# Performance work log

Measured on AMD Instinct MI355X. Metric: run time of the kernel, lower is better.

Reference implementation:

```python
import jax, jax.numpy as jnp
import numpy as np

B, S, E, H = 2, 2048, 1024, 16
DH = E // H
SCALE = DH ** -0.5

def setup_inputs() -> dict:
    key = jax.random.key(0)
    ks = jax.random.split(key, 5)
    w_std = (2.0 / (E + E)) ** 0.5  # xavier-ish scale
    return {
        'x': jax.random.normal(ks[0], (B, S, E), jnp.float32),
        'Wq': jax.random.normal(ks[1], (E, E), jnp.float32) * w_std,
        'bq': jnp.zeros((E,), jnp.float32),
        'Wk': jax.random.normal(ks[2], (E, E), jnp.float32) * w_std,
        'bk': jnp.zeros((E,), jnp.float32),
        'Wv': jax.random.normal(ks[3], (E, E), jnp.float32) * w_std,
        'bv': jnp.zeros((E,), jnp.float32),
        'Wo': jax.random.normal(ks[4], (E, E), jnp.float32) * w_std,
        'bo': jnp.zeros((E,), jnp.float32),
    }

def reference(x, Wq, bq, Wk, bk, Wv, bv, Wo, bo):
    # self-attention: query = key = value = x; torch Linear: y = x @ W.T + b
    q = (x @ Wq.T + bq) * SCALE            # [B,S,E]
    k = x @ Wk.T + bk
    v = x @ Wv.T + bv
    # split heads -> [B,S,H,DH]
    q = q.reshape(B, S, H, DH)
    k = k.reshape(B, S, H, DH)
    v = v.reshape(B, S, H, DH)
    # explicit attention matrix [B,H,S,S] (faithful to unfused bmm path)
    scores = jnp.einsum('bqhd,bkhd->bhqk', q, k)
    probs = jax.nn.softmax(scores, axis=-1)
    attn = jnp.einsum('bhqk,bkhd->bqhd', probs, v).reshape(B, S, E)
    return attn @ Wo.T + bo                # [B,S,E]
```

## Files before the change

kernel.cpp:

```cpp
#include <hip/hip_runtime.h>
#include <stdint.h>

#define BB 2
#define SS 2048
#define EE 1024
#define HH 16
#define DHD 64
#define MM (BB*SS)
#define QSCALE (0.125f * 1.4426950408889634f)

typedef __bf16 bf16;
typedef __bf16 bf16x8 __attribute__((ext_vector_type(8)));
typedef __bf16 bf16x4 __attribute__((ext_vector_type(4)));
typedef float  f32x4  __attribute__((ext_vector_type(4)));
typedef unsigned short ushort8 __attribute__((ext_vector_type(8)));

#define MFMA16(a,b,c) __builtin_amdgcn_mfma_f32_16x16x32_bf16(a,b,c,0,0,0)

__device__ __forceinline__ void gload_lds16(const void* g, void* l) {
  __builtin_amdgcn_global_load_lds(
      (const __attribute__((address_space(1))) unsigned int*)g,
      (__attribute__((address_space(3))) unsigned int*)l, 16, 0, 0);
}

__device__ __forceinline__ unsigned short f2bf(float f) {
  union { float f; unsigned u; } v; v.f = f;
  return (unsigned short)((v.u + 0x7FFFu + ((v.u >> 16) & 1u)) >> 16);
}

__global__ void convert_kernel(const float* __restrict__ x,
                               const float* __restrict__ wq, const float* __restrict__ wk,
                               const float* __restrict__ wv, const float* __restrict__ wo,
                               unsigned short* __restrict__ xbf,
                               unsigned short* __restrict__ wqb, unsigned short* __restrict__ wkb,
                               unsigned short* __restrict__ wvb, unsigned short* __restrict__ wob) {
  long t = (long)blockIdx.x * blockDim.x + threadIdx.x;
  long base = t * 8;
  const float* src; unsigned short* dst; long off;
  if (base < 4194304L) { src = x; dst = xbf; off = base; }
  else {
    long r = base - 4194304L; int j = (int)(r >> 20); off = r & 1048575L;
    src = (j==0)?wq:(j==1)?wk:(j==2)?wv:wo;
    dst = (j==0)?wqb:(j==1)?wkb:(j==2)?wvb:wob;
  }
  const float4* s4 = (const float4*)(src + off);
  float4 a = s4[0], b = s4[1];
  ushort8 o;
  o[0]=f2bf(a.x); o[1]=f2bf(a.y); o[2]=f2bf(a.z); o[3]=f2bf(a.w);
  o[4]=f2bf(b.x); o[5]=f2bf(b.y); o[6]=f2bf(b.z); o[7]=f2bf(b.w);
  *(ushort8*)(dst + off) = o;
}

#define G_STAGE(kbuf, kt) { \
    const size_t kb_ = (size_t)(kt) * 64; \
    char* d_ = lds + (kbuf) * 16384 + tid * 16; \
    gload_lds16(a0 + kb_, d_); \
    gload_lds16(a1 + kb_, d_ + 4096); \
    gload_lds16(b0 + kb_, d_ + 8192); \
    gload_lds16(b1 + kb_, d_ + 12288); \
  }

__global__ __launch_bounds__(256) void qkv_gemm(
    const bf16* __restrict__ xbf,
    const bf16* __restrict__ wqb, const bf16* __restrict__ wkb, const bf16* __restrict__ wvb,
    const float* __restrict__ bq, const float* __restrict__ bk, const float* __restrict__ bv,
    bf16* __restrict__ Q, bf16* __restrict__ K, bf16* __restrict__ VT) {
  __shared__ char lds[32768] __attribute__((aligned(16)));
  const int tid = threadIdx.x;
  const int bm = blockIdx.y * 128;
  const int bnG = blockIdx.x * 128;
  const int proj = bnG >> 10;
  const int bn = bnG & 1023;
  const bf16* wsel = (proj==0)?wqb:(proj==1)?wkb:wvb;
  const float* bias = (proj==0)?bq:(proj==1)?bk:bv;

  const int lane = tid & 63, w = tid >> 6;
  const int wm = (w>>1)*64, wn = (w&1)*64;
  const int c = lane & 15, g = lane >> 4;

  const int sr = tid >> 2;
  const int scb = ((tid & 3) * 16) ^ ((sr & 3) << 4);
  const char* a0 = (const char*)xbf  + ((size_t)(bm + sr     ) * 1024) * 2 + scb;
  const char* a1 = (const char*)xbf  + ((size_t)(bm + 64 + sr) * 1024) * 2 + scb;
  const char* b0 = (const char*)wsel + ((size_t)(bn + sr     ) * 1024) * 2 + scb;
  const char* b1 = (const char*)wsel + ((size_t)(bn + 64 + sr) * 1024) * 2 + scb;

  int aoff[4], boff[4];
#pragma unroll
  for (int mt=0; mt<4; ++mt) { int rr = wm + mt*16 + c; aoff[mt] = rr*64 + ((g*16) ^ ((rr&3)<<4)); }
#pragma unroll
  for (int nt=0; nt<4; ++nt) { int rr = wn + nt*16 + c; boff[nt] = 8192 + rr*64 + ((g*16) ^ ((rr&3)<<4)); }

  f32x4 acc[4][4];
#pragma unroll
  for (int mt=0; mt<4; ++mt)
#pragma unroll
    for (int nt=0; nt<4; ++nt) acc[mt][nt] = (f32x4){0.f,0.f,0.f,0.f};

  G_STAGE(0, 0);
  for (int kt = 0; kt < 32; ++kt) {
    const int cur = kt & 1;
    if (kt < 31) {
      G_STAGE(cur ^ 1, kt + 1);
      asm volatile("s_waitcnt vmcnt(4)" ::: "memory");
    } else {
      asm volatile("s_waitcnt vmcnt(0)" ::: "memory");
    }
    __builtin_amdgcn_s_barrier();
    const char* Ts = lds + cur * 16384;
    bf16x8 af[4], bfv[4];
#pragma unroll
    for (int mt=0; mt<4; ++mt) af[mt] = *(const bf16x8*)(Ts + aoff[mt]);
#pragma unroll
    for (int nt=0; nt<4; ++nt) bfv[nt] = *(const bf16x8*)(Ts + boff[nt]);
#pragma unroll
    for (int mt=0; mt<4; ++mt)
#pragma unroll
      for (int nt=0; nt<4; ++nt)
        acc[mt][nt] = MFMA16(af[mt], bfv[nt], acc[mt][nt]);
    asm volatile("s_waitcnt lgkmcnt(0)" ::: "memory");
    __builtin_amdgcn_s_barrier();
  }

  const int bidx = bm >> 11;
  const int srow = bm & 2047;
#pragma unroll
  for (int nt=0; nt<4; ++nt) {
    const int n = bn + wn + nt*16 + c;
    const float bv_ = bias[n];
    const int h = n >> 6, d = n & 63;
#pragma unroll
    for (int mt=0; mt<4; ++mt) {
      f32x4 a = acc[mt][nt];
      const int m0 = wm + mt*16 + g*4;
      if (proj == 0) {
#pragma unroll
        for (int r=0;r<4;++r) {
          int s = srow + m0 + r;
          Q[(((size_t)(bidx*16 + h))*2048 + s)*64 + d] = (bf16)((a[r] + bv_) * QSCALE);
        }
      } else if (proj == 1) {
#pragma unroll
        for (int r=0;r<4;++r) {
          int s = srow + m0 + r;
          K[(((size_t)(bidx*16 + h))*2048 + s)*64 + d] = (bf16)(a[r] + bv_);
        }
      } else {
        bf16x4 pk;
#pragma unroll
        for (int r=0;r<4;++r) pk[r] = (bf16)(a[r] + bv_);
        *(bf16x4*)(VT + (((size_t)(bidx*16 + h))*64 + d)*2048 + (srow + m0)) = pk;
      }
    }
  }
}

__global__ __launch_bounds__(256) void attn_kernel(
    const bf16* __restrict__ Q, const bf16* __restrict__ K,
    const bf16* __restrict__ VT, bf16* __restrict__ attn_out) {
  __shared__ char alds[32768] __attribute__((aligned(16)));
  const int tid = threadIdx.x;
  const int lane = tid & 63, w = tid >> 6;
  const int c = lane & 15, g = lane >> 4;
  const int x7 = c & 7;
  const int bh = blockIdx.y;
  const int qb = blockIdx.x * 64 + w * 16;
  const bf16* Qh = Q + (size_t)bh * 2048 * 64;
  const char* Khb = (const char*)(K  + (size_t)bh * 2048 * 64);
  const char* Vhb = (const char*)(VT + (size_t)bh * 64 * 2048);

  const int srow = tid >> 3, schunk = tid & 7;
  const int ssw = ((schunk ^ (srow & 7)) << 4);
  const char* srcK = Khb + (size_t)srow * 128  + ssw;
  const char* srcV = Vhb + (size_t)srow * 4096 + ssw;

#define ATT_STAGE(buf, kv) { \
    const char* sk_ = srcK + (size_t)(kv) * 128; \
    const char* sv_ = srcV + (size_t)(kv) * 2; \
    char* d_ = alds + (buf) * 16384 + tid * 16; \
    gload_lds16(sk_,            d_); \
    gload_lds16(sk_ + 32*128,   d_ + 4096); \
    gload_lds16(sv_,            d_ + 8192); \
    gload_lds16(sv_ + 32*4096,  d_ + 12288); \
  }

  bf16x8 qf0 = *(const bf16x8*)(Qh + (size_t)(qb + c)*64 + g*8);
  bf16x8 qf1 = *(const bf16x8*)(Qh + (size_t)(qb + c)*64 + 32 + g*8);

  f32x4 o[4];
#pragma unroll
  for (int dt=0; dt<4; ++dt) o[dt] = (f32x4){0.f,0.f,0.f,0.f};
  float m = -1e30f, l = 0.f;

  ATT_STAGE(0, 0);
  for (int t = 0; t < 32; ++t) {
    const int cur = t & 1;
    if (t < 31) {
      ATT_STAGE(cur ^ 1, (t + 1) * 64);
      asm volatile("s_waitcnt vmcnt(4)" ::: "memory");
    } else {
      asm volatile("s_waitcnt vmcnt(0)" ::: "memory");
    }
    __builtin_amdgcn_s_barrier();

    const char* Kl = alds + cur * 16384;
    const char* Vl = Kl + 8192;

    f32x4 st[4];
    __builtin_amdgcn_s_setprio(1);
#pragma unroll
    for (int ks = 0; ks < 4; ++ks) {
      const char* kr = Kl + (ks*16 + c) * 128;
      bf16x8 k0 = *(const bf16x8*)(kr + (((g    ) ^ x7) << 4));
      bf16x8 k1 = *(const bf16x8*)(kr + (((g + 4) ^ x7) << 4));
      f32x4 z = (f32x4){0.f,0.f,0.f,0.f};
      z = MFMA16(k0, qf0, z);
      z = MFMA16(k1, qf1, z);
      st[ks] = z;
    }
    __builtin_amdgcn_s_setprio(0);

    float m0_ = fmaxf(fmaxf(st[0][0], st[0][1]), st[0][2]);
    float m1_ = fmaxf(fmaxf(st[0][3], st[1][0]), st[1][1]);
    float m2_ = fmaxf(fmaxf(st[1][2], st[1][3]), st[2][0]);
    float m3_ = fmaxf(fmaxf(st[2][1], st[2][2]), st[2][3]);
    float m4_ = fmaxf(fmaxf(st[3][0], st[3][1]), st[3][2]);
    float tmax = fmaxf(fmaxf(fmaxf(m0_, m1_), m2_), fmaxf(fmaxf(m3_, m4_), st[3][3]));
    tmax = fmaxf(tmax, __shfl_xor(tmax, 16, 64));
    tmax = fmaxf(tmax, __shfl_xor(tmax, 32, 64));

    float p[4][4]; float ps = 0.f;
    if (__all(tmax <= m + 8.f)) {
#pragma unroll
      for (int ks = 0; ks < 4; ++ks)
#pragma unroll
        for (int r = 0; r < 4; ++r) { p[ks][r] = __builtin_exp2f(st[ks][r] - m); ps += p[ks][r]; }
      ps += __shfl_xor(ps, 16, 64);
      ps += __shfl_xor(ps, 32, 64);
      l += ps;
    } else {
      const float mnew = fmaxf(m, tmax);
      const float corr = __builtin_exp2f(m - mnew);
#pragma unroll
      for (int ks = 0; ks < 4; ++ks)
#pragma unroll
        for (int r = 0; r < 4; ++r) { p[ks][r] = __builtin_exp2f(st[ks][r] - mnew); ps += p[ks][r]; }
      ps += __shfl_xor(ps, 16, 64);
      ps += __shfl_xor(ps, 32, 64);
      l = l * corr + ps;
      m = mnew;
#pragma unroll
      for (int dt=0; dt<4; ++dt) o[dt] *= corr;
    }

    bf16x8 pfA, pfB;
#pragma unroll
    for (int r = 0; r < 4; ++r) {
      pfA[r] = (bf16)p[0][r]; pfA[4+r] = (bf16)p[1][r];
      pfB[r] = (bf16)p[2][r]; pfB[4+r] = (bf16)p[3][r];
    }

    const int i8 = (g & 1) * 8, gh = g >> 1;
    __builtin_amdgcn_s_setprio(1);
#pragma unroll
    for (int dt = 0; dt < 4; ++dt) {
      const char* vr = Vl + (dt*16 + c) * 128;
      bf16x4 va0 = *(const bf16x4*)(vr + (((gh    ) ^ x7) << 4) + i8);
      bf16x4 va1 = *(const bf16x4*)(vr + (((gh + 2) ^ x7) << 4) + i8);
      bf16x4 vb0 = *(const bf16x4*)(vr + (((gh + 4) ^ x7) << 4) + i8);
      bf16x4 vb1 = *(const bf16x4*)(vr + (((gh + 6) ^ x7) << 4) + i8);
      bf16x8 vfA = __builtin_shufflevector(va0, va1, 0,1,2,3,4,5,6,7);
      bf16x8 vfB = __builtin_shufflevector(vb0, vb1, 0,1,2,3,4,5,6,7);
      o[dt] = MFMA16(vfA, pfA, o[dt]);
      o[dt] = MFMA16(vfB, pfB, o[dt]);
    }
    __builtin_amdgcn_s_setprio(0);

    asm volatile("s_waitcnt lgkmcnt(0)" ::: "memory");
    __builtin_amdgcn_s_barrier();
  }
#undef ATT_STAGE

  const float inv = 1.0f / l;
  const int srow_q = qb + c;
  const int b = bh >> 4, h = bh & 15;
  bf16* outrow = attn_out + ((size_t)(b*2048 + srow_q))*1024 + h*64;
#pragma unroll
  for (int dt=0; dt<4; ++dt) {
    bf16x4 ov;
#pragma unroll
    for (int r=0;r<4;++r) ov[r] = (bf16)(o[dt][r] * inv);
    *(bf16x4*)(outrow + dt*16 + g*4) = ov;
  }
}

__global__ __launch_bounds__(256) void out_gemm(
    const bf16* __restrict__ A, const bf16* __restrict__ W,
    const float* __restrict__ bias, float* __restrict__ out) {
  __shared__ char lds[32768] __attribute__((aligned(16)));
  const int tid = threadIdx.x;
  const int bm = blockIdx.y * 128, bn = blockIdx.x * 128;
  const int lane = tid & 63, w = tid >> 6;
  const int wm = (w>>1)*64, wn = (w&1)*64;
  const int c = lane & 15, g = lane >> 4;

  const int sr = tid >> 2;
  const int scb = ((tid & 3) * 16) ^ ((sr & 3) << 4);
  const char* a0 = (const char*)A + ((size_t)(bm + sr     ) * 1024) * 2 + scb;
  const char* a1 = (const char*)A + ((size_t)(bm + 64 + sr) * 1024) * 2 + scb;
  const char* b0 = (const char*)W + ((size_t)(bn + sr     ) * 1024) * 2 + scb;
  const char* b1 = (const char*)W + ((size_t)(bn + 64 + sr) * 1024) * 2 + scb;

  int aoff[4], boff[4];
#pragma unroll
  for (int mt=0; mt<4; ++mt) { int rr = wm + mt*16 + c; aoff[mt] = rr*64 + ((g*16) ^ ((rr&3)<<4)); }
#pragma unroll
  for (int nt=0; nt<4; ++nt) { int rr = wn + nt*16 + c; boff[nt] = 8192 + rr*64 + ((g*16) ^ ((rr&3)<<4)); }

  f32x4 acc[4][4];
#pragma unroll
  for (int mt=0; mt<4; ++mt)
#pragma unroll
    for (int nt=0; nt<4; ++nt) acc[mt][nt] = (f32x4){0.f,0.f,0.f,0.f};

  G_STAGE(0, 0);
  for (int kt = 0; kt < 32; ++kt) {
    const int cur = kt & 1;
    if (kt < 31) {
      G_STAGE(cur ^ 1, kt + 1);
      asm volatile("s_waitcnt vmcnt(4)" ::: "memory");
    } else {
      asm volatile("s_waitcnt vmcnt(0)" ::: "memory");
    }
    __builtin_amdgcn_s_barrier();
    const char* Ts = lds + cur * 16384;
    bf16x8 af[4], bfv[4];
#pragma unroll
    for (int mt=0; mt<4; ++mt) af[mt] = *(const bf16x8*)(Ts + aoff[mt]);
#pragma unroll
    for (int nt=0; nt<4; ++nt) bfv[nt] = *(const bf16x8*)(Ts + boff[nt]);
#pragma unroll
    for (int mt=0; mt<4; ++mt)
#pragma unroll
      for (int nt=0; nt<4; ++nt)
        acc[mt][nt] = MFMA16(af[mt], bfv[nt], acc[mt][nt]);
    asm volatile("s_waitcnt lgkmcnt(0)" ::: "memory");
    __builtin_amdgcn_s_barrier();
  }

#pragma unroll
  for (int nt=0; nt<4; ++nt) {
    const int n = bn + wn + nt*16 + c;
    const float bv_ = bias[n];
#pragma unroll
    for (int mt=0; mt<4; ++mt) {
      const int m0 = bm + wm + mt*16 + g*4;
#pragma unroll
      for (int r=0;r<4;++r) out[(size_t)(m0 + r)*1024 + n] = acc[mt][nt][r] + bv_;
    }
  }
}

extern "C" void kernel_launch(void* const* d_in, const int* in_sizes, int n_in,
                              void* d_out, int out_size, void* d_ws, size_t ws_size,
                              hipStream_t stream) {
  const float* x  = (const float*)d_in[0];
  const float* Wq = (const float*)d_in[1];
  const float* bq = (const float*)d_in[2];
  const float* Wk = (const float*)d_in[3];
  const float* bk = (const float*)d_in[4];
  const float* Wv = (const float*)d_in[5];
  const float* bv = (const float*)d_in[6];
  const float* Wo = (const float*)d_in[7];
  const float* bo = (const float*)d_in[8];

  char* ws = (char*)d_ws;
  const size_t MiB = 1u << 20;
  unsigned short* xbf = (unsigned short*)(ws);
  unsigned short* wqb = (unsigned short*)(ws +  8*MiB);
  unsigned short* wkb = (unsigned short*)(ws + 10*MiB);
  unsigned short* wvb = (unsigned short*)(ws + 12*MiB);
  unsigned short* wob = (unsigned short*)(ws + 14*MiB);
  bf16* Qb    = (bf16*)(ws + 16*MiB);
  bf16* Kb    = (bf16*)(ws + 24*MiB);
  bf16* VTb   = (bf16*)(ws + 32*MiB);
  bf16* attnb = (bf16*)(ws + 40*MiB);

  convert_kernel<<<4096, 256, 0, stream>>>(x, Wq, Wk, Wv, Wo, xbf, wqb, wkb, wvb, wob);
  qkv_gemm<<<dim3(24, 32), 256, 0, stream>>>(
      (const bf16*)xbf, (const bf16*)wqb, (const bf16*)wkb, (const bf16*)wvb,
      bq, bk, bv, Qb, Kb, VTb);
  attn_kernel<<<dim3(32, 32), 256, 0, stream>>>(Qb, Kb, VTb, attnb);
  out_gemm<<<dim3(8, 32), 256, 0, stream>>>(attnb, (const bf16*)wob, bo, (float*)d_out);
}
```

Measured before the change: 239.5 us.

## Swap MFMA operands for vectorized Q/K/out stores; simplify online softmax

Swapping the A/B operands of the MFMA in the Q/K projection and output GEMMs transposes the accumulator layout, so each lane holds four consecutive columns. That allows packed bf16x4 stores for Q/K and float4 stores for the output, with float4 bias loads, instead of scattered scalar stores. The attention kernel drops the lazy-rescale branch and always rescales, and removes the s_setprio hints. The K-loop is factored into a shared template. The unconditional rescale adds multiply work per tile, and removing setprio may change how waves interleave.

```diff
diff --git a/kernel.cpp b/kernel.cpp
--- a/kernel.cpp
+++ b/kernel.cpp
@@ -51,7 +51,7 @@
   *(ushort8*)(dst + off) = o;
 }
 
-#define G_STAGE(kbuf, kt) { \
+#define GS_STAGE(kbuf, kt) { \
     const size_t kb_ = (size_t)(kt) * 64; \
     char* d_ = lds + (kbuf) * 16384 + tid * 16; \
     gload_lds16(a0 + kb_, d_); \
@@ -59,6 +59,38 @@
     gload_lds16(b0 + kb_, d_ + 8192); \
     gload_lds16(b1 + kb_, d_ + 12288); \
   }
+
+template<bool SWAP>
+__device__ __forceinline__ void gemm_kloop(
+    const char* a0, const char* a1, const char* b0, const char* b1,
+    char* lds, const int tid, const int (&aoff)[4], const int (&boff)[4],
+    f32x4 (&acc)[4][4]) {
+  GS_STAGE(0, 0);
+  for (int kt = 0; kt < 32; ++kt) {
+    const int cur = kt & 1;
+    if (kt < 31) {
+      GS_STAGE(cur ^ 1, kt + 1);
+      asm volatile("s_waitcnt vmcnt(4)" ::: "memory");
+    } else {
+      asm volatile("s_waitcnt vmcnt(0)" ::: "memory");
+    }
+    __builtin_amdgcn_s_barrier();
+    const char* Ts = lds + cur * 16384;
+    bf16x8 af[4], bfv[4];
+#pragma unroll
+    for (int mt=0; mt<4; ++mt) af[mt] = *(const bf16x8*)(Ts + aoff[mt]);
+#pragma unroll
+    for (int nt=0; nt<4; ++nt) bfv[nt] = *(const bf16x8*)(Ts + boff[nt]);
+#pragma unroll
+    for (int mt=0; mt<4; ++mt)
+#pragma unroll
+      for (int nt=0; nt<4; ++nt)
+        acc[mt][nt] = SWAP ? MFMA16(bfv[nt], af[mt], acc[mt][nt])
+                           : MFMA16(af[mt], bfv[nt], acc[mt][nt]);
+    asm volatile("s_waitcnt lgkmcnt(0)" ::: "memory");
+    __builtin_amdgcn_s_barrier();
+  }
+}
 
 __global__ __launch_bounds__(256) void qkv_gemm(
     const bf16* __restrict__ xbf,
@@ -97,58 +129,42 @@
 #pragma unroll
     for (int nt=0; nt<4; ++nt) acc[mt][nt] = (f32x4){0.f,0.f,0.f,0.f};
 
-  G_STAGE(0, 0);
-  for (int kt = 0; kt < 32; ++kt) {
-    const int cur = kt & 1;
-    if (kt < 31) {
-      G_STAGE(cur ^ 1, kt + 1);
-      asm volatile("s_waitcnt vmcnt(4)" ::: "memory");
-    } else {
-      asm volatile("s_waitcnt vmcnt(0)" ::: "memory");
-    }
-    __builtin_amdgcn_s_barrier();
-    const char* Ts = lds + cur * 16384;
-    bf16x8 af[4], bfv[4];
-#pragma unroll
-    for (int mt=0; mt<4; ++mt) af[mt] = *(const bf16x8*)(Ts + aoff[mt]);
-#pragma unroll
-    for (int nt=0; nt<4; ++nt) bfv[nt] = *(const bf16x8*)(Ts + boff[nt]);
-#pragma unroll
-    for (int mt=0; mt<4; ++mt)
-#pragma unroll
-      for (int nt=0; nt<4; ++nt)
-        acc[mt][nt] = MFMA16(af[mt], bfv[nt], acc[mt][nt]);
-    asm volatile("s_waitcnt lgkmcnt(0)" ::: "memory");
-    __builtin_amdgcn_s_barrier();
-  }
-
   const int bidx = bm >> 11;
   const int srow = bm & 2047;
-#pragma unroll
-  for (int nt=0; nt<4; ++nt) {
-    const int n = bn + wn + nt*16 + c;
-    const float bv_ = bias[n];
-    const int h = n >> 6, d = n & 63;
-#pragma unroll
-    for (int mt=0; mt<4; ++mt) {
-      f32x4 a = acc[mt][nt];
-      const int m0 = wm + mt*16 + g*4;
-      if (proj == 0) {
-#pragma unroll
-        for (int r=0;r<4;++r) {
-          int s = srow + m0 + r;
-          Q[(((size_t)(bidx*16 + h))*2048 + s)*64 + d] = (bf16)((a[r] + bv_) * QSCALE);
-        }
-      } else if (proj == 1) {
-#pragma unroll
-        for (int r=0;r<4;++r) {
-          int s = srow + m0 + r;
-          K[(((size_t)(bidx*16 + h))*2048 + s)*64 + d] = (bf16)(a[r] + bv_);
-        }
-      } else {
+
+  if (proj != 2) {
+    gemm_kloop<true>(a0, a1, b0, b1, lds, tid, aoff, boff, acc);
+    bf16* dst = (proj == 0) ? Q : K;
+    const float qs = (proj == 0) ? QSCALE : 1.0f;
+#pragma unroll
+    for (int nt=0; nt<4; ++nt) {
+      const int n0 = bn + wn + nt*16 + g*4;
+      const float4 b4 = *(const float4*)(bias + n0);
+      const int h = n0 >> 6, d0 = n0 & 63;
+#pragma unroll
+      for (int mt=0; mt<4; ++mt) {
+        const int s = srow + wm + mt*16 + c;
         bf16x4 pk;
-#pragma unroll
-        for (int r=0;r<4;++r) pk[r] = (bf16)(a[r] + bv_);
+        pk[0] = (bf16)((acc[mt][nt][0] + b4.x) * qs);
+        pk[1] = (bf16)((acc[mt][nt][1] + b4.y) * qs);
+        pk[2] = (bf16)((acc[mt][nt][2] + b4.z) * qs);
+        pk[3] = (bf16)((acc[mt][nt][3] + b4.w) * qs);
+        *(bf16x4*)(dst + (((size_t)(bidx*16 + h))*2048 + s)*64 + d0) = pk;
+      }
+    }
+  } else {
+    gemm_kloop<false>(a0, a1, b0, b1, lds, tid, aoff, boff, acc);
+#pragma unroll
+    for (int nt=0; nt<4; ++nt) {
+      const int n = bn + wn + nt*16 + c;
+      const float bv_ = bias[n];
+      const int h = n >> 6, d = n & 63;
+#pragma unroll
+      for (int mt=0; mt<4; ++mt) {
+        const int m0 = wm + mt*16 + g*4;
+        bf16x4 pk;
+#pragma unroll
+        for (int r=0;r<4;++r) pk[r] = (bf16)(acc[mt][nt][r] + bv_);
         *(bf16x4*)(VT + (((size_t)(bidx*16 + h))*64 + d)*2048 + (srow + m0)) = pk;
       }
     }
@@ -207,7 +223,6 @@
     const char* Vl = Kl + 8192;
 
     f32x4 st[4];
-    __builtin_amdgcn_s_setprio(1);
 #pragma unroll
     for (int ks = 0; ks < 4; ++ks) {
       const char* kr = Kl + (ks*16 + c) * 128;
@@ -218,40 +233,26 @@
       z = MFMA16(k1, qf1, z);
       st[ks] = z;
     }
-    __builtin_amdgcn_s_setprio(0);
-
-    float m0_ = fmaxf(fmaxf(st[0][0], st[0][1]), st[0][2]);
-    float m1_ = fmaxf(fmaxf(st[0][3], st[1][0]), st[1][1]);
-    float m2_ = fmaxf(fmaxf(st[1][2], st[1][3]), st[2][0]);
-    float m3_ = fmaxf(fmaxf(st[2][1], st[2][2]), st[2][3]);
-    float m4_ = fmaxf(fmaxf(st[3][0], st[3][1]), st[3][2]);
-    float tmax = fmaxf(fmaxf(fmaxf(m0_, m1_), m2_), fmaxf(fmaxf(m3_, m4_), st[3][3]));
+
+    float tmax = -1e30f;
+#pragma unroll
+    for (int ks = 0; ks < 4; ++ks)
+      tmax = fmaxf(tmax, fmaxf(fmaxf(st[ks][0], st[ks][1]), fmaxf(st[ks][2], st[ks][3])));
     tmax = fmaxf(tmax, __shfl_xor(tmax, 16, 64));
     tmax = fmaxf(tmax, __shfl_xor(tmax, 32, 64));
-
+    const float mnew = fmaxf(m, tmax);
+    const float corr = __builtin_exp2f(m - mnew);
     float p[4][4]; float ps = 0.f;
-    if (__all(tmax <= m + 8.f)) {
-#pragma unroll
-      for (int ks = 0; ks < 4; ++ks)
-#pragma unroll
-        for (int r = 0; r < 4; ++r) { p[ks][r] = __builtin_exp2f(st[ks][r] - m); ps += p[ks][r]; }
-      ps += __shfl_xor(ps, 16, 64);
-      ps += __shfl_xor(ps, 32, 64);
-      l += ps;
-    } else {
-      const float mnew = fmaxf(m, tmax);
-      const float corr = __builtin_exp2f(m - mnew);
-#pragma unroll
-      for (int ks = 0; ks < 4; ++ks)
-#pragma unroll
-        for (int r = 0; r < 4; ++r) { p[ks][r] = __builtin_exp2f(st[ks][r] - mnew); ps += p[ks][r]; }
-      ps += __shfl_xor(ps, 16, 64);
-      ps += __shfl_xor(ps, 32, 64);
-      l = l * corr + ps;
-      m = mnew;
-#pragma unroll
-      for (int dt=0; dt<4; ++dt) o[dt] *= corr;
-    }
+#pragma unroll
+    for (int ks = 0; ks < 4; ++ks)
+#pragma unroll
+      for (int r = 0; r < 4; ++r) { p[ks][r] = __builtin_exp2f(st[ks][r] - mnew); ps += p[ks][r]; }
+    ps += __shfl_xor(ps, 16, 64);
+    ps += __shfl_xor(ps, 32, 64);
+    l = l * corr + ps;
+    m = mnew;
+#pragma unroll
+    for (int dt=0; dt<4; ++dt) o[dt] *= corr;
 
     bf16x8 pfA, pfB;
 #pragma unroll
@@ -260,11 +261,10 @@
       pfB[r] = (bf16)p[2][r]; pfB[4+r] = (bf16)p[3][r];
     }
 
-    const int i8 = (g & 1) * 8, gh = g >> 1;
-    __builtin_amdgcn_s_setprio(1);
 #pragma unroll
     for (int dt = 0; dt < 4; ++dt) {
       const char* vr = Vl + (dt*16 + c) * 128;
+      const int i8 = (g & 1) * 8, gh = g >> 1;
       bf16x4 va0 = *(const bf16x4*)(vr + (((gh    ) ^ x7) << 4) + i8);
       bf16x4 va1 = *(const bf16x4*)(vr + (((gh + 2) ^ x7) << 4) + i8);
       bf16x4 vb0 = *(const bf16x4*)(vr + (((gh + 4) ^ x7) << 4) + i8);
@@ -274,7 +274,6 @@
       o[dt] = MFMA16(vfA, pfA, o[dt]);
       o[dt] = MFMA16(vfB, pfB, o[dt]);
     }
-    __builtin_amdgcn_s_setprio(0);
 
     asm volatile("s_waitcnt lgkmcnt(0)" ::: "memory");
     __builtin_amdgcn_s_barrier();
@@ -323,40 +322,21 @@
 #pragma unroll
     for (int nt=0; nt<4; ++nt) acc[mt][nt] = (f32x4){0.f,0.f,0.f,0.f};
 
-  G_STAGE(0, 0);
-  for (int kt = 0; kt < 32; ++kt) {
-    const int cur = kt & 1;
-    if (kt < 31) {
-      G_STAGE(cur ^ 1, kt + 1);
-      asm volatile("s_waitcnt vmcnt(4)" ::: "memory");
-    } else {
-      asm volatile("s_waitcnt vmcnt(0)" ::: "memory");
-    }
-    __builtin_amdgcn_s_barrier();
-    const char* Ts = lds + cur * 16384;
-    bf16x8 af[4], bfv[4];
-#pragma unroll
-    for (int mt=0; mt<4; ++mt) af[mt] = *(const bf16x8*)(Ts + aoff[mt]);
-#pragma unroll
-    for (int nt=0; nt<4; ++nt) bfv[nt] = *(const bf16x8*)(Ts + boff[nt]);
-#pragma unroll
-    for (int mt=0; mt<4; ++mt)
-#pragma unroll
-      for (int nt=0; nt<4; ++nt)
-        acc[mt][nt] = MFMA16(af[mt], bfv[nt], acc[mt][nt]);
-    asm volatile("s_waitcnt lgkmcnt(0)" ::: "memory");
-    __builtin_amdgcn_s_barrier();
-  }
+  gemm_kloop<true>(a0, a1, b0, b1, lds, tid, aoff, boff, acc);
 
 #pragma unroll
   for (int nt=0; nt<4; ++nt) {
-    const int n = bn + wn + nt*16 + c;
-    const float bv_ = bias[n];
+    const int n0 = bn + wn + nt*16 + g*4;
+    const float4 b4 = *(const float4*)(bias + n0);
 #pragma unroll
     for (int mt=0; mt<4; ++mt) {
-      const int m0 = bm + wm + mt*16 + g*4;
-#pragma unroll
-      for (int r=0;r<4;++r) out[(size_t)(m0 + r)*1024 + n] = acc[mt][nt][r] + bv_;
+      const int m0 = bm + wm + mt*16 + c;
+      float4 ov;
+      ov.x = acc[mt][nt][0] + b4.x;
+      ov.y = acc[mt][nt][1] + b4.y;
+      ov.z = acc[mt][nt][2] + b4.z;
+      ov.w = acc[mt][nt][3] + b4.w;
+      *(float4*)(out + (size_t)m0*1024 + n0) = ov;
     }
   }
 }
```

Result: faster. 233.0 us (-2.7%).
